# Kernel tuning notes

Measured on AMD Instinct MI355X. Metric: run time of the kernel, lower is better.

The kernel has to match this reference:

```python
import jax, jax.numpy as jnp
import numpy as np

N_NODES = 100000
D_FEAT = 128
N_EDGES = 300000
HIDDEN = 64


def setup_inputs() -> dict:
    key = jax.random.key(0)
    k1, k2, k3, k4 = jax.random.split(key, 4)
    node_emb = jax.random.normal(k1, (N_NODES, D_FEAT), dtype=jnp.float32)
    train_sample = jax.random.randint(k2, (N_EDGES, 2), 0, N_NODES, dtype=jnp.int64)
    input_dim = 2 * D_FEAT
    r1 = np.sqrt(6.0 / input_dim)
    w1 = jax.random.uniform(k3, (input_dim, HIDDEN), minval=-r1, maxval=r1, dtype=jnp.float32)
    b1 = jnp.zeros((HIDDEN,), dtype=jnp.float32)
    r2 = np.sqrt(6.0 / HIDDEN)
    w2 = jax.random.uniform(k4, (HIDDEN, 1), minval=-r2, maxval=r2, dtype=jnp.float32)
    return {"input": node_emb, "train_sample": train_sample, "w1": w1, "b1": b1, "w2": w2}


def reference(input, train_sample, w1, b1, w2):
    # gather source/target node embeddings: [E, D] each
    src = input[train_sample[:, 0]]
    dst = input[train_sample[:, 1]]
    h = jnp.concatenate([src, dst], axis=1)  # [E, 2D]
    x = jax.nn.relu(h @ w1 + b1)             # [E, HIDDEN]
    return x @ w2                             # [E, 1]
```

## Files before the change

kernel.cpp:

```cpp
#include <hip/hip_runtime.h>
#include <hip/hip_bf16.h>


#define D_FEAT 128
#define HIDDEN 64

typedef __attribute__((ext_vector_type(8))) short v8s;
typedef __attribute__((ext_vector_type(4))) float f32x4;

__device__ inline unsigned short f2bf(float f) {
    unsigned u = __builtin_bit_cast(unsigned, f);
    unsigned r = (u + 0x7FFFu + ((u >> 16) & 1u)) >> 16;
    return (unsigned short)r;
}
__device__ inline float bf2f(unsigned short u) {
    return __builtin_bit_cast(float, (unsigned)u << 16);
}

__device__ inline bool detect_is64(const int* ts32, int lane) {
    int probe = ts32[2 * lane + 1];
    return __ballot(probe != 0) == 0ULL;
}

__global__ void __launch_bounds__(256, 4)
precompute_kernel(const float* __restrict__ emb, const float* __restrict__ w1,
                  const float* __restrict__ b1, unsigned short* __restrict__ P,
                  int n_nodes) {
    __shared__ unsigned short bt[16384];
    const int t    = threadIdx.x;
    const int lane = t & 63;
    const int wid  = t >> 6;
    const int sub  = lane & 15;
    const int g    = lane >> 4;
    const int m0   = blockIdx.x * 64 + wid * 16;

    int arow = m0 + sub;
    if (arow >= n_nodes) arow = n_nodes - 1;
    const float* aptr = emb + (size_t)arow * D_FEAT + g * 8;
    float4 a[8];
#pragma unroll
    for (int ks = 0; ks < 4; ++ks) {
        a[2 * ks]     = *reinterpret_cast<const float4*>(aptr + ks * 32);
        a[2 * ks + 1] = *reinterpret_cast<const float4*>(aptr + ks * 32 + 4);
    }

    {
        const int k    = t & 127;
        const int half = t >> 7;
        const float4* src = reinterpret_cast<const float4*>(w1 + (size_t)t * 64);
#pragma unroll
        for (int j4 = 0; j4 < 16; ++j4) {
            const float4 v = src[j4];
            const int cb = half * 64 + j4 * 4;
            bt[((cb + 0) * 128 + k) ^ (((cb + 0) & 7) << 3)] = f2bf(v.x);
            bt[((cb + 1) * 128 + k) ^ (((cb + 1) & 7) << 3)] = f2bf(v.y);
            bt[((cb + 2) * 128 + k) ^ (((cb + 2) & 7) << 3)] = f2bf(v.z);
            bt[((cb + 3) * 128 + k) ^ (((cb + 3) & 7) << 3)] = f2bf(v.w);
        }
    }
    __syncthreads();

    f32x4 acc[8];
#pragma unroll
    for (int nj = 0; nj < 8; ++nj) acc[nj] = (f32x4){0.f, 0.f, 0.f, 0.f};

#pragma unroll
    for (int ks = 0; ks < 4; ++ks) {
        const int k0 = ks * 32;
        const float4 a0 = a[2 * ks], a1 = a[2 * ks + 1];
        v8s af;
        af[0] = (short)f2bf(a0.x); af[1] = (short)f2bf(a0.y);
        af[2] = (short)f2bf(a0.z); af[3] = (short)f2bf(a0.w);
        af[4] = (short)f2bf(a1.x); af[5] = (short)f2bf(a1.y);
        af[6] = (short)f2bf(a1.z); af[7] = (short)f2bf(a1.w);
#pragma unroll
        for (int nj = 0; nj < 8; ++nj) {
            const int c = nj * 16 + sub;
            const int eidx = (c * 128 + k0 + g * 8) ^ ((c & 7) << 3);
            const v8s bf = *reinterpret_cast<const v8s*>(&bt[eidx]);
            acc[nj] = __builtin_amdgcn_mfma_f32_16x16x32_bf16(bf, af, acc[nj], 0, 0, 0);
        }
    }

    float4 bias[4];
#pragma unroll
    for (int nj = 0; nj < 4; ++nj)
        bias[nj] = *reinterpret_cast<const float4*>(b1 + nj * 16 + g * 4);

    const int node = m0 + sub;
    if (node < n_nodes) {
#pragma unroll
        for (int nj = 0; nj < 8; ++nj) {
            float b0 = 0.f, b1v = 0.f, b2 = 0.f, b3 = 0.f;
            if (nj < 4) { b0 = bias[nj].x; b1v = bias[nj].y;
                          b2 = bias[nj].z; b3 = bias[nj].w; }
            ushort4 o;
            o.x = f2bf(acc[nj][0] + b0);
            o.y = f2bf(acc[nj][1] + b1v);
            o.z = f2bf(acc[nj][2] + b2);
            o.w = f2bf(acc[nj][3] + b3);
            *reinterpret_cast<ushort4*>(P + (size_t)node * 128 + nj * 16 + g * 4) = o;
        }
    }
}

__device__ inline float pairterm(unsigned aw, unsigned bw, float w0, float w1) {
    float a0 = __builtin_bit_cast(float, aw << 16);
    float a1 = __builtin_bit_cast(float, aw & 0xFFFF0000u);
    float b0 = __builtin_bit_cast(float, bw << 16);
    float b1 = __builtin_bit_cast(float, bw & 0xFFFF0000u);
    float h0 = a0 + b0; h0 = h0 > 0.f ? h0 : 0.f;
    float h1 = a1 + b1; h1 = h1 > 0.f ? h1 : 0.f;
    return h0 * w0 + h1 * w1;
}

__global__ void __launch_bounds__(256)
edge_kernel(const unsigned short* __restrict__ P, const void* __restrict__ ts,
            const float* __restrict__ w2, float* __restrict__ out, int n_edges) {
    const int lane = threadIdx.x & 63;
    const int wid  = threadIdx.x >> 6;
    const int sub  = lane & 7;
    const int grp  = lane >> 3;
    const int gw   = blockIdx.x * 4 + wid;
    const int nw   = gridDim.x * 4;

    const int* ts32 = (const int*)ts;
    const long long* ts64 = (const long long*)ts;
    const bool is64 = detect_is64(ts32, lane);

    const float4 w2a = *reinterpret_cast<const float4*>(w2 + sub * 8);
    const float4 w2b = *reinterpret_cast<const float4*>(w2 + sub * 8 + 4);

    for (int e = gw * 8 + grp; e < n_edges; e += nw * 8) {
        long long s, d;
        if (is64) { s = ts64[2 * e]; d = ts64[2 * e + 1]; }
        else      { s = ts32[2 * e]; d = ts32[2 * e + 1]; }
        const uint4 a = *reinterpret_cast<const uint4*>(P + (size_t)s * 128 + sub * 8);
        const uint4 b = *reinterpret_cast<const uint4*>(P + (size_t)d * 128 + 64 + sub * 8);
        float v = pairterm(a.x, b.x, w2a.x, w2a.y)
                + pairterm(a.y, b.y, w2a.z, w2a.w)
                + pairterm(a.z, b.z, w2b.x, w2b.y)
                + pairterm(a.w, b.w, w2b.z, w2b.w);
#pragma unroll
        for (int off = 1; off < 8; off <<= 1) v += __shfl_xor(v, off);
        if (sub == 0) out[e] = v;
    }
}

__global__ void __launch_bounds__(256)
direct_kernel(const float* __restrict__ emb, const void* __restrict__ ts,
              const float* __restrict__ w1, const float* __restrict__ b1,
              const float* __restrict__ w2, float* __restrict__ out, int n_edges) {
    const int lane = threadIdx.x & 63;
    const int gw   = blockIdx.x * (blockDim.x >> 6) + (threadIdx.x >> 6);
    const int nw   = gridDim.x * (blockDim.x >> 6);
    const float w2v  = w2[lane];
    const float bias = b1[lane];
    const int* ts32 = (const int*)ts;
    const long long* ts64 = (const long long*)ts;
    const bool is64 = detect_is64(ts32, lane);

    for (int e = gw; e < n_edges; e += nw) {
        long long s, d;
        if (is64) { s = ts64[2 * e]; d = ts64[2 * e + 1]; }
        else      { s = ts32[2 * e]; d = ts32[2 * e + 1]; }
        const float4* s4 = reinterpret_cast<const float4*>(emb + s * D_FEAT);
        const float4* d4 = reinterpret_cast<const float4*>(emb + d * D_FEAT);
        float acc = bias;
#pragma unroll
        for (int k4 = 0; k4 < 32; ++k4) {
            float4 r = s4[k4];
            acc += r.x * w1[(4 * k4 + 0) * 64 + lane];
            acc += r.y * w1[(4 * k4 + 1) * 64 + lane];
            acc += r.z * w1[(4 * k4 + 2) * 64 + lane];
            acc += r.w * w1[(4 * k4 + 3) * 64 + lane];
        }
#pragma unroll
        for (int k4 = 0; k4 < 32; ++k4) {
            float4 r = d4[k4];
            acc += r.x * w1[(128 + 4 * k4 + 0) * 64 + lane];
            acc += r.y * w1[(128 + 4 * k4 + 1) * 64 + lane];
            acc += r.z * w1[(128 + 4 * k4 + 2) * 64 + lane];
            acc += r.w * w1[(128 + 4 * k4 + 3) * 64 + lane];
        }
        float h = acc > 0.0f ? acc : 0.0f;
        float v = h * w2v;
#pragma unroll
        for (int off = 32; off > 0; off >>= 1) v += __shfl_xor(v, off);
        if (lane == 0) out[e] = v;
    }
}

extern "C" void kernel_launch(void* const* d_in, const int* in_sizes, int n_in,
                              void* d_out, int out_size, void* d_ws, size_t ws_size,
                              hipStream_t stream) {
    const float* emb = (const float*)d_in[0];
    const void*  ts  = d_in[1];
    const float* w1  = (const float*)d_in[2];
    const float* b1  = (const float*)d_in[3];
    const float* w2  = (const float*)d_in[4];
    float* out = (float*)d_out;

    const int n_nodes = in_sizes[0] / D_FEAT;
    const int n_edges = in_sizes[1] / 2;

    const size_t p_bytes = (size_t)n_nodes * 128 * sizeof(unsigned short);

    if (ws_size >= p_bytes) {
        unsigned short* P = (unsigned short*)d_ws;
        const int nblocks = (n_nodes + 63) / 64;
        precompute_kernel<<<nblocks, 256, 0, stream>>>(emb, w1, b1, P, n_nodes);
        edge_kernel<<<2048, 256, 0, stream>>>(P, ts, w2, out, n_edges);
    } else {
        direct_kernel<<<2048, 256, 0, stream>>>(emb, ts, w1, b1, w2, out, n_edges);
    }
}
```

Measured before the change: 45.89 us.

## Make precompute kernel persistent with double-buffered row prefetch

The precompute GEMM kernel now runs on a fixed grid of 1024 blocks. Each wave loops over 16-row tiles in a grid-stride pattern and prefetches the next tile's embedding rows into registers while the current tile runs its MFMAs. Before, each block converted all of W1 to bf16 in LDS but used it for only 64 nodes; now that setup is spread over many more tiles. The cost is higher register pressure from the second buffer, and the launch-bounds occupancy hint is dropped.

```diff
diff --git a/kernel.cpp b/kernel.cpp
--- a/kernel.cpp
+++ b/kernel.cpp
@@ -13,16 +13,13 @@
     unsigned r = (u + 0x7FFFu + ((u >> 16) & 1u)) >> 16;
     return (unsigned short)r;
 }
-__device__ inline float bf2f(unsigned short u) {
-    return __builtin_bit_cast(float, (unsigned)u << 16);
-}
 
 __device__ inline bool detect_is64(const int* ts32, int lane) {
     int probe = ts32[2 * lane + 1];
     return __ballot(probe != 0) == 0ULL;
 }
 
-__global__ void __launch_bounds__(256, 4)
+__global__ void __launch_bounds__(256)
 precompute_kernel(const float* __restrict__ emb, const float* __restrict__ w1,
                   const float* __restrict__ b1, unsigned short* __restrict__ P,
                   int n_nodes) {
@@ -32,17 +29,6 @@
     const int wid  = t >> 6;
     const int sub  = lane & 15;
     const int g    = lane >> 4;
-    const int m0   = blockIdx.x * 64 + wid * 16;
-
-    int arow = m0 + sub;
-    if (arow >= n_nodes) arow = n_nodes - 1;
-    const float* aptr = emb + (size_t)arow * D_FEAT + g * 8;
-    float4 a[8];
-#pragma unroll
-    for (int ks = 0; ks < 4; ++ks) {
-        a[2 * ks]     = *reinterpret_cast<const float4*>(aptr + ks * 32);
-        a[2 * ks + 1] = *reinterpret_cast<const float4*>(aptr + ks * 32 + 4);
-    }
 
     {
         const int k    = t & 127;
@@ -58,49 +44,75 @@
             bt[((cb + 3) * 128 + k) ^ (((cb + 3) & 7) << 3)] = f2bf(v.w);
         }
     }
-    __syncthreads();
-
-    f32x4 acc[8];
-#pragma unroll
-    for (int nj = 0; nj < 8; ++nj) acc[nj] = (f32x4){0.f, 0.f, 0.f, 0.f};
-
-#pragma unroll
-    for (int ks = 0; ks < 4; ++ks) {
-        const int k0 = ks * 32;
-        const float4 a0 = a[2 * ks], a1 = a[2 * ks + 1];
-        v8s af;
-        af[0] = (short)f2bf(a0.x); af[1] = (short)f2bf(a0.y);
-        af[2] = (short)f2bf(a0.z); af[3] = (short)f2bf(a0.w);
-        af[4] = (short)f2bf(a1.x); af[5] = (short)f2bf(a1.y);
-        af[6] = (short)f2bf(a1.z); af[7] = (short)f2bf(a1.w);
-#pragma unroll
-        for (int nj = 0; nj < 8; ++nj) {
-            const int c = nj * 16 + sub;
-            const int eidx = (c * 128 + k0 + g * 8) ^ ((c & 7) << 3);
-            const v8s bf = *reinterpret_cast<const v8s*>(&bt[eidx]);
-            acc[nj] = __builtin_amdgcn_mfma_f32_16x16x32_bf16(bf, af, acc[nj], 0, 0, 0);
-        }
-    }
 
     float4 bias[4];
 #pragma unroll
     for (int nj = 0; nj < 4; ++nj)
         bias[nj] = *reinterpret_cast<const float4*>(b1 + nj * 16 + g * 4);
 
-    const int node = m0 + sub;
-    if (node < n_nodes) {
-#pragma unroll
-        for (int nj = 0; nj < 8; ++nj) {
-            float b0 = 0.f, b1v = 0.f, b2 = 0.f, b3 = 0.f;
-            if (nj < 4) { b0 = bias[nj].x; b1v = bias[nj].y;
-                          b2 = bias[nj].z; b3 = bias[nj].w; }
-            ushort4 o;
-            o.x = f2bf(acc[nj][0] + b0);
-            o.y = f2bf(acc[nj][1] + b1v);
-            o.z = f2bf(acc[nj][2] + b2);
-            o.w = f2bf(acc[nj][3] + b3);
-            *reinterpret_cast<ushort4*>(P + (size_t)node * 128 + nj * 16 + g * 4) = o;
-        }
+    __syncthreads();
+
+    const int ntiles = (n_nodes + 15) / 16;
+    const int gwave  = blockIdx.x * 4 + wid;
+    const int nwave  = gridDim.x * 4;
+
+    auto loadA = [&](float4* a, int tt) {
+        int row = tt * 16 + sub;
+        if (row >= n_nodes) row = n_nodes - 1;
+        const float* p = emb + (size_t)row * D_FEAT + g * 8;
+#pragma unroll
+        for (int ks = 0; ks < 4; ++ks) {
+            a[2 * ks]     = *reinterpret_cast<const float4*>(p + ks * 32);
+            a[2 * ks + 1] = *reinterpret_cast<const float4*>(p + ks * 32 + 4);
+        }
+    };
+
+    float4 A0[8], A1[8];
+    if (gwave < ntiles) loadA(A0, gwave);
+
+    for (int tt = gwave; tt < ntiles; tt += nwave) {
+        const int tn = tt + nwave;
+        if (tn < ntiles) loadA(A1, tn);
+        f32x4 acc[8];
+#pragma unroll
+        for (int nj = 0; nj < 8; ++nj) acc[nj] = (f32x4){0.f, 0.f, 0.f, 0.f};
+
+#pragma unroll
+        for (int ks = 0; ks < 4; ++ks) {
+            const int k0 = ks * 32;
+            const float4 a0 = A0[2 * ks], a1 = A0[2 * ks + 1];
+            v8s af;
+            af[0] = (short)f2bf(a0.x); af[1] = (short)f2bf(a0.y);
+            af[2] = (short)f2bf(a0.z); af[3] = (short)f2bf(a0.w);
+            af[4] = (short)f2bf(a1.x); af[5] = (short)f2bf(a1.y);
+            af[6] = (short)f2bf(a1.z); af[7] = (short)f2bf(a1.w);
+#pragma unroll
+            for (int nj = 0; nj < 8; ++nj) {
+                const int c = nj * 16 + sub;
+                const int eidx = (c * 128 + k0 + g * 8) ^ ((c & 7) << 3);
+                const v8s bf = *reinterpret_cast<const v8s*>(&bt[eidx]);
+                acc[nj] = __builtin_amdgcn_mfma_f32_16x16x32_bf16(bf, af, acc[nj], 0, 0, 0);
+            }
+        }
+
+        const int node = tt * 16 + sub;
+        if (node < n_nodes) {
+#pragma unroll
+            for (int nj = 0; nj < 8; ++nj) {
+                float b0 = 0.f, b1v = 0.f, b2 = 0.f, b3 = 0.f;
+                if (nj < 4) { b0 = bias[nj].x; b1v = bias[nj].y;
+                              b2 = bias[nj].z; b3 = bias[nj].w; }
+                ushort4 o;
+                o.x = f2bf(acc[nj][0] + b0);
+                o.y = f2bf(acc[nj][1] + b1v);
+                o.z = f2bf(acc[nj][2] + b2);
+                o.w = f2bf(acc[nj][3] + b3);
+                *reinterpret_cast<ushort4*>(P + (size_t)node * 128 + nj * 16 + g * 4) = o;
+            }
+        }
+
+#pragma unroll
+        for (int i = 0; i < 8; ++i) A0[i] = A1[i];
     }
 }
 
@@ -208,8 +220,7 @@
 
     if (ws_size >= p_bytes) {
         unsigned short* P = (unsigned short*)d_ws;
-        const int nblocks = (n_nodes + 63) / 64;
-        precompute_kernel<<<nblocks, 256, 0, stream>>>(emb, w1, b1, P, n_nodes);
+        precompute_kernel<<<1024, 256, 0, stream>>>(emb, w1, b1, P, n_nodes);
         edge_kernel<<<2048, 256, 0, stream>>>(P, ts, w2, out, n_edges);
     } else {
         direct_kernel<<<2048, 256, 0, stream>>>(emb, ts, w1, b1, w2, out, n_edges);
```

New measurement: 39.56 us. -13.8%, faster.
